# Kernel tuning notes

Measured on AMD Instinct MI355X. Metric: run time of the kernel, lower is better.

Reference implementation:

```python
import jax, jax.numpy as jnp
import numpy as np

N_USERS = 100000
M_ITEMS = 200000
N_NODES = N_USERS + M_ITEMS
N_EDGES = 1200000
D = 64
N_LAYERS = 3
BATCH = 4096


def setup_inputs() -> dict:
    key = jax.random.key(0)
    ks = jax.random.split(key, 11)
    return {
        "users": jax.random.randint(ks[0], (BATCH,), 0, N_USERS),
        "items": jax.random.randint(ks[1], (BATCH,), 0, M_ITEMS),
        "rows": jax.random.randint(ks[2], (N_EDGES,), 0, N_NODES),
        "cols": jax.random.randint(ks[3], (N_EDGES,), 0, N_NODES),
        "vals": jax.random.uniform(ks[4], (N_EDGES,), dtype=jnp.float32),
        "user_emb": jax.random.normal(ks[5], (N_USERS, D), dtype=jnp.float32) * 0.1,
        "item_emb": jax.random.normal(ks[6], (M_ITEMS, D), dtype=jnp.float32) * 0.1,
        "W_gc": jax.random.normal(ks[7], (N_LAYERS, D, D), dtype=jnp.float32) * 0.1,
        "b_gc": jax.random.normal(ks[8], (N_LAYERS, D), dtype=jnp.float32) * 0.1,
        "W_bi": jax.random.normal(ks[9], (N_LAYERS, D, D), dtype=jnp.float32) * 0.1,
        "b_bi": jax.random.normal(ks[10], (N_LAYERS, D), dtype=jnp.float32) * 0.1,
    }


def _spmm(rows, cols, vals, x):
    # sparse.mm(Graph, x): out[r] = sum_e vals[e] * x[cols[e]] for rows[e]==r
    gathered = vals[:, None] * x[cols]  # [E, D]
    return jax.ops.segment_sum(gathered, rows, num_segments=N_NODES)


def _computer(rows, cols, vals, user_emb, item_emb, W_gc, b_gc, W_bi, b_bi):
    ego = jnp.concatenate([user_emb, item_emb], axis=0)  # [N, D]
    embs = [ego]
    for k in range(N_LAYERS):
        side = _spmm(rows, cols, vals, ego)
        sum_emb = side @ W_gc[k] + b_gc[k]
        bi_emb = (ego * side) @ W_bi[k] + b_bi[k]
        ego = jax.nn.leaky_relu(sum_emb + bi_emb, negative_slope=0.2)
        nrm = jnp.linalg.norm(ego, axis=1, keepdims=True)
        ego = ego / jnp.maximum(nrm, 1e-12)
        embs.append(ego)
    mean_emb = jnp.mean(jnp.stack(embs, axis=1), axis=1)  # [N, D]
    return mean_emb[:N_USERS], mean_emb[N_USERS:]


def reference(users, items, rows, cols, vals, user_emb, item_emb, W_gc, b_gc, W_bi, b_bi):
    all_users, all_items = _computer(rows, cols, vals, user_emb, item_emb, W_gc, b_gc, W_bi, b_bi)
    u = all_users[users]  # [B, D]
    i = all_items[items]  # [B, D]
    return jnp.sum(u * i, axis=1)  # [B]
```

## Files before the change

kernel.cpp:

```cpp
#include <hip/hip_runtime.h>
#include <hip/hip_bf16.h>

#define N_USERS 100000
#define M_ITEMS 200000
#define N_NODES 300000
#define N_EDGES 1200000
#define BATCH   4096
#define NB      ((N_NODES + 255) / 256)
#define CHUNK   5

typedef __attribute__((ext_vector_type(8))) short short8;
typedef __attribute__((ext_vector_type(4))) float floatx4;

static __device__ __forceinline__ float b2f(__hip_bfloat16 x) { return __bfloat162float(x); }

static __device__ __forceinline__ short f2bs(float f) {
    union { __hip_bfloat16 h; short s; } u;
    u.h = __float2bfloat16(f);
    return u.s;
}
static __device__ __forceinline__ float us2f(unsigned int us) {
    return __uint_as_float(us << 16);
}

static __device__ __forceinline__ float loadf(const void* p, int i, int isbf) {
    if (isbf) return b2f(((const __hip_bfloat16*)p)[i]);
    return ((const float*)p)[i];
}

static __device__ __forceinline__ void unpack8(float* o, uint4 e) {
    unsigned int w[4] = {e.x, e.y, e.z, e.w};
#pragma unroll
    for (int j = 0; j < 8; ++j) o[j] = us2f((w[j >> 1] >> ((j & 1) * 16)) & 0xFFFFu);
}

static __device__ __forceinline__ void gather16(
    float* o0, float* o1, const unsigned short* ego,
    const void* ue, const void* ie, int node, int quad, int isbf, int use_src) {
    if (!use_src) {
        const unsigned short* p = ego + (size_t)node * 64 + quad * 8;
        unpack8(o0, *(const uint4*)p);
        unpack8(o1, *(const uint4*)(p + 32));
    } else if (isbf) {
        const unsigned short* p = (node < N_USERS)
            ? (const unsigned short*)ue + (size_t)node * 64
            : (const unsigned short*)ie + (size_t)(node - N_USERS) * 64;
        p += quad * 8;
        unpack8(o0, *(const uint4*)p);
        unpack8(o1, *(const uint4*)(p + 32));
    } else {
        const float* p = (node < N_USERS)
            ? (const float*)ue + (size_t)node * 64
            : (const float*)ie + (size_t)(node - N_USERS) * 64;
        p += quad * 8;
        float4 a = *(const float4*)p;
        float4 b = *(const float4*)(p + 4);
        float4 c = *(const float4*)(p + 32);
        float4 d = *(const float4*)(p + 36);
        o0[0]=a.x; o0[1]=a.y; o0[2]=a.z; o0[3]=a.w; o0[4]=b.x; o0[5]=b.y; o0[6]=b.z; o0[7]=b.w;
        o1[0]=c.x; o1[1]=c.y; o1[2]=c.z; o1[3]=c.w; o1[4]=d.x; o1[5]=d.y; o1[6]=d.z; o1[7]=d.w;
    }
}

__global__ void sniff_kernel(const unsigned short* __restrict__ v16, int* __restrict__ flag) {
    if (blockIdx.x == 0 && threadIdx.x == 0) {
        int c = 0;
        for (int i = 0; i < 16; ++i) {
            unsigned int ub = (v16[2 * i] >> 8) & 0xFF;
            if (ub >= 0x3A && ub <= 0x3F) ++c;
        }
        *flag = (c >= 12) ? 1 : 0;
    }
}

__global__ __launch_bounds__(256) void wtrans_kernel(
    const void* __restrict__ Wg, const void* __restrict__ bg,
    const void* __restrict__ Wb, const void* __restrict__ bb,
    const int* __restrict__ flagp, unsigned short* __restrict__ WT,
    float* __restrict__ sb) {
    int isbf = __builtin_amdgcn_readfirstlane(flagp[0]);
    int t = blockIdx.x * 256 + threadIdx.x;
    if (t < 3072) {
        int lane = t & 63, h = (t >> 6) & 1, ct = (t >> 7) & 3, w = (t >> 9) & 1, k = t >> 10;
        int m = lane & 15, quad = lane >> 4;
        const void* Wsrc = w ? Wb : Wg;
#pragma unroll
        for (int j = 0; j < 8; ++j) {
            int kk = h * 32 + quad * 8 + j;
            WT[(size_t)(k * 1024 + w * 512 + ct * 128 + h * 64 + lane) * 8 + j] =
                (unsigned short)f2bs(loadf(Wsrc, k * 4096 + kk * 64 + ct * 16 + m, isbf));
        }
    }
    if (t < 192) sb[t] = loadf(bg, t, isbf) + loadf(bb, t, isbf);
}

__global__ __launch_bounds__(256) void seed_kernel(
    const int* __restrict__ users, const int* __restrict__ items,
    unsigned char* __restrict__ f1, unsigned char* __restrict__ f2,
    unsigned char* __restrict__ f3) {
    int i = blockIdx.x * 256 + threadIdx.x;
    int n = -1;
    if (i < BATCH) n = users[i];
    else if (i < 2 * BATCH) n = N_USERS + items[i - BATCH];
    if (n >= 0) { f1[n] = 1; f2[n] = 1; f3[n] = 1; }
}

__global__ __launch_bounds__(256) void prop1_count_kernel(
    const int4* __restrict__ rows4, const int4* __restrict__ cols4,
    const unsigned char* __restrict__ src, unsigned char* __restrict__ dst,
    int* __restrict__ off) {
    int t = blockIdx.x * 256 + threadIdx.x;
    if (t < N_EDGES / 4) {
        int4 r = rows4[t];
        int4 c = cols4[t];
        atomicAdd(&off[r.x + 1], 1);
        atomicAdd(&off[r.y + 1], 1);
        atomicAdd(&off[r.z + 1], 1);
        atomicAdd(&off[r.w + 1], 1);
        if (src[r.x]) dst[c.x] = 1;
        if (src[r.y]) dst[c.y] = 1;
        if (src[r.z]) dst[c.z] = 1;
        if (src[r.w]) dst[c.w] = 1;
    }
}

__global__ __launch_bounds__(256) void prop_kernel(
    const int4* __restrict__ rows4, const int4* __restrict__ cols4,
    const unsigned char* __restrict__ src, unsigned char* __restrict__ dst) {
    int t = blockIdx.x * 256 + threadIdx.x;
    if (t < N_EDGES / 4) {
        int4 r = rows4[t];
        int4 c = cols4[t];
        if (src[r.x]) dst[c.x] = 1;
        if (src[r.y]) dst[c.y] = 1;
        if (src[r.z]) dst[c.z] = 1;
        if (src[r.w]) dst[c.w] = 1;
    }
}

static __device__ __forceinline__ int deg_class(int d) {
    return d >= 16 ? 0 : d >= 8 ? 1 : d >= 4 ? 2 : 3;
}

__global__ __launch_bounds__(256) void cblock_count12_kernel(
    const unsigned char* __restrict__ flags, const int* __restrict__ off,
    int* __restrict__ bcnt) {
    __shared__ int w[4];
    int n = blockIdx.x * 256 + threadIdx.x;
    int lane = threadIdx.x & 63;
    int wid  = threadIdx.x >> 6;
    bool ir = (n < N_NODES);
    int cls = 3;
    if (ir) cls = deg_class(off[n + 1] - off[n]);
#pragma unroll
    for (int L = 0; L < 3; ++L) {
        bool fl = ir && flags[L * N_NODES + n];
#pragma unroll
        for (int c = 0; c < 4; ++c) {
            unsigned long long mask = __ballot(fl && (cls == c));
            if (lane == 0) w[wid] = __popcll(mask);
            __syncthreads();
            if (threadIdx.x == 0) bcnt[(L * 4 + c) * NB + blockIdx.x] = w[0] + w[1] + w[2] + w[3];
            __syncthreads();
        }
    }
}

__global__ __launch_bounds__(256) void cscan_top12_kernel(
    int* __restrict__ bcnt, int* __restrict__ cnts) {
    __shared__ int s[256];
    int t = threadIdx.x;
    for (int L = 0; L < 3; ++L) {
        int levelRun = 0;
        for (int c = 0; c < 4; ++c) {
            int v = L * 4 + c;
            int base = t * CHUNK;
            int loc = 0;
            for (int j = 0; j < CHUNK; ++j) { int i = base + j; if (i < NB) loc += bcnt[v * NB + i]; }
            s[t] = loc;
            __syncthreads();
            for (int o = 1; o < 256; o <<= 1) {
                int add = (t >= o) ? s[t - o] : 0;
                __syncthreads();
                s[t] += add;
                __syncthreads();
            }
            int run = ((t == 0) ? 0 : s[t - 1]) + levelRun;
            int total = s[255];
            for (int j = 0; j < CHUNK; ++j) {
                int i = base + j;
                if (i < NB) { int tmp = bcnt[v * NB + i]; bcnt[v * NB + i] = run; run += tmp; }
            }
            levelRun += total;
            __syncthreads();
        }
        if (t == 0) cnts[L] = levelRun;
    }
}

__global__ __launch_bounds__(256) void cscatter12_kernel(
    const unsigned char* __restrict__ flags, const int* __restrict__ off,
    const int* __restrict__ bcnt, int* __restrict__ lists) {
    __shared__ int wsum[4];
    int n = blockIdx.x * 256 + threadIdx.x;
    int lane = threadIdx.x & 63;
    int wid  = threadIdx.x >> 6;
    bool ir = (n < N_NODES);
    int cls = 3;
    if (ir) cls = deg_class(off[n + 1] - off[n]);
#pragma unroll
    for (int L = 0; L < 3; ++L) {
        bool fl = ir && flags[L * N_NODES + n];
#pragma unroll
        for (int c = 0; c < 4; ++c) {
            bool f = fl && (cls == c);
            unsigned long long mask = __ballot(f);
            if (lane == 0) wsum[wid] = __popcll(mask);
            __syncthreads();
            int base = bcnt[(L * 4 + c) * NB + blockIdx.x];
            for (int i = 0; i < wid; ++i) base += wsum[i];
            if (f) {
                int pos = base + __popcll(mask & ((1ull << lane) - 1ull));
                lists[L * N_NODES + pos] = n;
            }
            __syncthreads();
        }
    }
}

__global__ __launch_bounds__(256) void scan_bsum_kernel(
    const int* __restrict__ A, int* __restrict__ bsum) {
    __shared__ int s[256];
    int t = threadIdx.x;
    int i = blockIdx.x * 256 + t;
    s[t] = (i < N_NODES) ? A[i] : 0;
    __syncthreads();
    for (int o = 128; o >= 1; o >>= 1) {
        if (t < o) s[t] += s[t + o];
        __syncthreads();
    }
    if (t == 0) bsum[blockIdx.x] = s[0];
}

__global__ __launch_bounds__(256) void scan_top_kernel(int* __restrict__ bsum) {
    __shared__ int s[256];
    int t = threadIdx.x;
    int base = t * CHUNK;
    int loc = 0;
    for (int j = 0; j < CHUNK; ++j) { int i = base + j; if (i < NB) loc += bsum[i]; }
    s[t] = loc;
    __syncthreads();
    for (int o = 1; o < 256; o <<= 1) {
        int add = (t >= o) ? s[t - o] : 0;
        __syncthreads();
        s[t] += add;
        __syncthreads();
    }
    int run = (t == 0) ? 0 : s[t - 1];
    for (int j = 0; j < CHUNK; ++j) {
        int i = base + j;
        if (i < NB) { int tmp = bsum[i]; bsum[i] = run; run += tmp; }
    }
}

__global__ __launch_bounds__(256) void scan_block_kernel(
    int* __restrict__ A, const int* __restrict__ bsum, int* __restrict__ cursor) {
    __shared__ int s[256];
    int t = threadIdx.x;
    int i = blockIdx.x * 256 + t;
    s[t] = (i < N_NODES) ? A[i] : 0;
    __syncthreads();
    for (int o = 1; o < 256; o <<= 1) {
        int add = (t >= o) ? s[t - o] : 0;
        __syncthreads();
        s[t] += add;
        __syncthreads();
    }
    if (i < N_NODES) {
        int val = s[t] + bsum[blockIdx.x];
        A[i] = val;
        cursor[i + 1] = val;
    }
    if (blockIdx.x == 0 && t == 0) cursor[0] = 0;
}

__global__ __launch_bounds__(256) void fill_kernel(
    const int4* __restrict__ rows4, const int4* __restrict__ cols4,
    const void* __restrict__ vals, int* __restrict__ cursor,
    int2* __restrict__ epack, const int* __restrict__ flagp,
    const unsigned char* __restrict__ flag1) {
    int isbf = __builtin_amdgcn_readfirstlane(flagp[0]);
    int t = blockIdx.x * 256 + threadIdx.x;
    if (t < N_EDGES / 4) {
        int4 r = rows4[t];
        int4 c = cols4[t];
        int e = t * 4;
        if (flag1[r.x]) {
            int p = atomicAdd(&cursor[r.x], 1);
            epack[p] = make_int2(c.x, __float_as_int(loadf(vals, e, isbf)));
        }
        if (flag1[r.y]) {
            int p = atomicAdd(&cursor[r.y], 1);
            epack[p] = make_int2(c.y, __float_as_int(loadf(vals, e + 1, isbf)));
        }
        if (flag1[r.z]) {
            int p = atomicAdd(&cursor[r.z], 1);
            epack[p] = make_int2(c.z, __float_as_int(loadf(vals, e + 2, isbf)));
        }
        if (flag1[r.w]) {
            int p = atomicAdd(&cursor[r.w], 1);
            epack[p] = make_int2(c.w, __float_as_int(loadf(vals, e + 3, isbf)));
        }
    }
}

__global__ __launch_bounds__(256) void fused_layer_kernel(
    const int* __restrict__ off, const int2* __restrict__ epack,
    const unsigned short* __restrict__ ego_in,
    const void* __restrict__ ue, const void* __restrict__ ie,
    const unsigned short* __restrict__ WT, const float* __restrict__ sb,
    int klayer, unsigned short* __restrict__ ego_out,
    const int* __restrict__ flagp, const int* __restrict__ list,
    const int* __restrict__ cntp, int use_src) {
    const int isbf = __builtin_amdgcn_readfirstlane(flagp[0]);
    const int cnt  = __builtin_amdgcn_readfirstlane(cntp[0]);
    const int ntile = (cnt + 15) >> 4;
    const int lane = threadIdx.x & 63;
    const int m    = lane & 15;
    const int quad = lane >> 4;

    const unsigned short* wt = WT + (size_t)klayer * 8192;
    short8 Bg[4][2], Bb[4][2];
#pragma unroll
    for (int ct = 0; ct < 4; ++ct)
#pragma unroll
        for (int h = 0; h < 2; ++h) {
            Bg[ct][h] = *(const short8*)(wt + (size_t)((ct * 2 + h) * 64 + lane) * 8);
            Bb[ct][h] = *(const short8*)(wt + (size_t)(512 + (ct * 2 + h) * 64 + lane) * 8);
        }
    float bv[4];
#pragma unroll
    for (int ct = 0; ct < 4; ++ct) bv[ct] = sb[klayer * 64 + ct * 16 + m];

    const int wv = blockIdx.x * 4 + (threadIdx.x >> 6);
    const int nw = gridDim.x * 4;
    for (int tile = wv; tile < ntile; tile += nw) {
        const int idx = tile * 16 + m;
        const int row = list[idx < cnt ? idx : cnt - 1];
        const int start = off[row];
        const int end   = off[row + 1];

        float eg0[8], eg1[8];
        gather16(eg0, eg1, ego_in, ue, ie, row, quad, isbf, use_src);

        float s0[8] = {0,0,0,0,0,0,0,0};
        float s1[8] = {0,0,0,0,0,0,0,0};
        for (int e = start; e < end; ++e) {
            int2 cv = epack[e];
            float v = __int_as_float(cv.y);
            float t0[8], t1[8];
            gather16(t0, t1, ego_in, ue, ie, cv.x, quad, isbf, use_src);
#pragma unroll
            for (int j = 0; j < 8; ++j) {
                s0[j] = fmaf(v, t0[j], s0[j]);
                s1[j] = fmaf(v, t1[j], s1[j]);
            }
        }

        short8 As0, As1, Ap0, Ap1;
#pragma unroll
        for (int j = 0; j < 8; ++j) {
            As0[j] = f2bs(s0[j]);
            As1[j] = f2bs(s1[j]);
            Ap0[j] = f2bs(eg0[j] * s0[j]);
            Ap1[j] = f2bs(eg1[j] * s1[j]);
        }

        floatx4 acc[4];
#pragma unroll
        for (int ct = 0; ct < 4; ++ct) {
            floatx4 a = {0.f, 0.f, 0.f, 0.f};
            a = __builtin_amdgcn_mfma_f32_16x16x32_bf16(As0, Bg[ct][0], a, 0, 0, 0);
            a = __builtin_amdgcn_mfma_f32_16x16x32_bf16(As1, Bg[ct][1], a, 0, 0, 0);
            a = __builtin_amdgcn_mfma_f32_16x16x32_bf16(Ap0, Bb[ct][0], a, 0, 0, 0);
            a = __builtin_amdgcn_mfma_f32_16x16x32_bf16(Ap1, Bb[ct][1], a, 0, 0, 0);
            acc[ct] = a;
        }

        float v[4][4];
        float ssq[4] = {0.f, 0.f, 0.f, 0.f};
#pragma unroll
        for (int ct = 0; ct < 4; ++ct)
#pragma unroll
            for (int r = 0; r < 4; ++r) {
                float x = acc[ct][r] + bv[ct];
                x = x > 0.f ? x : 0.2f * x;
                v[ct][r] = x;
                ssq[r] += x * x;
            }
#pragma unroll
        for (int o = 1; o < 16; o <<= 1)
#pragma unroll
            for (int r = 0; r < 4; ++r) ssq[r] += __shfl_xor(ssq[r], o, 64);
#pragma unroll
        for (int r = 0; r < 4; ++r) {
            int idx_w = tile * 16 + quad * 4 + r;
            if (idx_w < cnt) {
                float sc = 1.0f / fmaxf(sqrtf(ssq[r]), 1e-12f);
                int rw = list[idx_w];
#pragma unroll
                for (int ct = 0; ct < 4; ++ct)
                    ego_out[(size_t)rw * 64 + ct * 16 + m] = (unsigned short)f2bs(v[ct][r] * sc);
            }
        }
    }
}

__global__ __launch_bounds__(256) void batch_acc_kernel(
    const int* __restrict__ users, const int* __restrict__ items,
    const unsigned short* __restrict__ ego, float* __restrict__ acc) {
    int gid = blockIdx.x * 256 + threadIdx.x;
    int b = gid >> 6;
    int lane = gid & 63;
    int node = (b < BATCH) ? users[b] : (N_USERS + items[b - BATCH]);
    acc[gid] += us2f(ego[(size_t)node * 64 + lane]);
}

__global__ __launch_bounds__(256) void dot_kernel(
    const int* __restrict__ users, const int* __restrict__ items,
    const float* __restrict__ acc, const void* __restrict__ ue,
    const void* __restrict__ ie, void* __restrict__ out,
    const int* __restrict__ flagp) {
    int isbf = __builtin_amdgcn_readfirstlane(flagp[0]);
    int gid = blockIdx.x * 256 + threadIdx.x;
    int b = gid >> 6;
    int lane = gid & 63;
    int un = __builtin_amdgcn_readfirstlane(users[b]);
    int in = __builtin_amdgcn_readfirstlane(items[b]);
    float u = acc[b * 64 + lane] + loadf(ue, un * 64 + lane, isbf);
    float v = acc[(BATCH + b) * 64 + lane] + loadf(ie, in * 64 + lane, isbf);
    float pr = u * v;
#pragma unroll
    for (int o = 32; o >= 1; o >>= 1) pr += __shfl_xor(pr, o, 64);
    if (lane == 0) {
        float r = pr * 0.0625f;
        if (isbf) ((__hip_bfloat16*)out)[b] = __float2bfloat16(r);
        else      ((float*)out)[b] = r;
    }
}

static inline size_t align16(size_t x) { return (x + 15) & ~(size_t)15; }

extern "C" void kernel_launch(void* const* d_in, const int* in_sizes, int n_in,
                              void* d_out, int out_size, void* d_ws, size_t ws_size,
                              hipStream_t stream) {
    const int* users = (const int*)d_in[0];
    const int* items = (const int*)d_in[1];
    const int* rows  = (const int*)d_in[2];
    const int* cols  = (const int*)d_in[3];
    const void* vals     = d_in[4];
    const void* user_emb = d_in[5];
    const void* item_emb = d_in[6];
    const void* W_gc     = d_in[7];
    const void* b_gc     = d_in[8];
    const void* W_bi     = d_in[9];
    const void* b_bi     = d_in[10];

    const size_t egoB   = (size_t)N_NODES * 64 * sizeof(short);
    const size_t packB  = (size_t)N_EDGES * sizeof(int2);
    const size_t curB   = (size_t)(N_NODES + 1) * sizeof(int);
    const size_t bsumB  = (size_t)NB * sizeof(int);
    const size_t bcntB  = (size_t)12 * NB * sizeof(int);
    const size_t wtB    = (size_t)3 * 1024 * 8 * sizeof(short);
    const size_t sbB    = (size_t)192 * sizeof(float);
    const size_t accB   = (size_t)2 * BATCH * 64 * sizeof(float);
    const size_t offB   = (size_t)(N_NODES + 1) * sizeof(int);
    const size_t flagsB = (size_t)3 * N_NODES;

    char* ws = (char*)d_ws;
    size_t o = 0;
    unsigned short* egoA  = (unsigned short*)(ws + o); o += egoB;
    unsigned short* egoB2 = (unsigned short*)(ws + o); o += egoB;
    int2*  epack  = (int2*)(ws + o);  o += packB;
    int*   cursor = (int*)(ws + o);   o += curB;
    int*   bsum   = (int*)(ws + o);   o += bsumB;
    int*   bcnt   = (int*)(ws + o);   o += bcntB;
    o = align16(o);
    unsigned short* WT = (unsigned short*)(ws + o); o += wtB;
    float* sb     = (float*)(ws + o); o += sbB;
    o = align16(o);
    float* acc    = (float*)(ws + o);
    int*   off    = (int*)((char*)acc + accB);
    int*   cnts   = (int*)((char*)off + offB);
    int*   flag   = cnts + 3;
    unsigned char* flags = (unsigned char*)(flag + 1);
    const size_t zeroB = accB + offB + 4 * sizeof(int) + flagsB;
    unsigned char* flagL[3] = {flags, flags + N_NODES, flags + 2 * N_NODES};
    int* lists = (int*)(flags + flagsB);
    int* listL[3] = {lists, lists + N_NODES, lists + 2 * N_NODES};

    hipMemsetAsync(acc, 0, zeroB, stream);
    sniff_kernel<<<1, 64, 0, stream>>>((const unsigned short*)vals, flag);
    wtrans_kernel<<<12, 256, 0, stream>>>(W_gc, b_gc, W_bi, b_bi, flag, WT, sb);

    seed_kernel<<<(2 * BATCH + 255) / 256, 256, 0, stream>>>(users, items, flagL[0], flagL[1], flagL[2]);
    prop1_count_kernel<<<(N_EDGES / 4 + 255) / 256, 256, 0, stream>>>(
        (const int4*)rows, (const int4*)cols, flagL[2], flagL[1], off);
    scan_bsum_kernel<<<NB, 256, 0, stream>>>(off + 1, bsum);
    scan_top_kernel<<<1, 256, 0, stream>>>(bsum);
    scan_block_kernel<<<NB, 256, 0, stream>>>(off + 1, bsum, cursor);
    prop_kernel<<<(N_EDGES / 4 + 255) / 256, 256, 0, stream>>>(
        (const int4*)rows, (const int4*)cols, flagL[1], flagL[0]);

    cblock_count12_kernel<<<NB, 256, 0, stream>>>(flags, off, bcnt);
    cscan_top12_kernel<<<1, 256, 0, stream>>>(bcnt, cnts);
    cscatter12_kernel<<<NB, 256, 0, stream>>>(flags, off, bcnt, lists);

    fill_kernel<<<(N_EDGES / 4 + 255) / 256, 256, 0, stream>>>(
        (const int4*)rows, (const int4*)cols, vals, cursor, epack, flag, flagL[0]);

    unsigned short* eg_in[3]  = {egoA, egoA, egoB2};
    unsigned short* eg_out[3] = {egoA, egoB2, egoA};
    for (int k = 0; k < 3; ++k) {
        int use_src = (k == 0) ? 1 : 0;
        fused_layer_kernel<<<2048, 256, 0, stream>>>(off, epack, eg_in[k], user_emb, item_emb,
                                                     WT, sb, k, eg_out[k],
                                                     flag, listL[k], cnts + k, use_src);
        batch_acc_kernel<<<(2 * BATCH * 64) / 256, 256, 0, stream>>>(users, items, eg_out[k], acc);
    }
    dot_kernel<<<(BATCH * 64) / 256, 256, 0, stream>>>(users, items, acc, user_emb, item_emb, d_out, flag);
}
```

Measured before the change: 344.7 us.

## Restructure CSR build with atomic ranks, fuse scans, fold batch accumulation into layers

Merges the sniff, weight-transpose and seed kernels into one setup kernel, and recomputes the dtype sniff inline where it is needed. Row counting now runs after the 2-hop propagation and only for flagged rows. It records each edge's atomic rank, so the fill kernel can scatter without a second round of atomics. The three scans are fused with the degree-class counting into three kernels. Per-batch accumulation is moved into the layer kernel through a map3 index, which removes three batch_acc launches but assumes batch rows are unique per node in map3 and packs ranks into 16 bits.

After: 309.5 us. 1.11x faster.

```diff
diff --git a/kernel.cpp b/kernel.cpp
--- a/kernel.cpp
+++ b/kernel.cpp
@@ -8,6 +8,8 @@
 #define BATCH   4096
 #define NB      ((N_NODES + 255) / 256)
 #define CHUNK   5
+#define EPT2    (N_EDGES / 2)
+#define EGRID   ((EPT2 + 255) / 256)
 
 typedef __attribute__((ext_vector_type(8))) short short8;
 typedef __attribute__((ext_vector_type(4))) float floatx4;
@@ -26,6 +28,17 @@
 static __device__ __forceinline__ float loadf(const void* p, int i, int isbf) {
     if (isbf) return b2f(((const __hip_bfloat16*)p)[i]);
     return ((const float*)p)[i];
+}
+
+static __device__ __forceinline__ int sniff_dev(const void* vals) {
+    const unsigned short* v16 = (const unsigned short*)vals;
+    int c = 0;
+#pragma unroll
+    for (int i = 0; i < 16; ++i) {
+        unsigned int ub = (v16[2 * i] >> 8) & 0xFF;
+        if (ub >= 0x3A && ub <= 0x3F) ++c;
+    }
+    return (c >= 12) ? 1 : 0;
 }
 
 static __device__ __forceinline__ void unpack8(float* o, uint4 e) {
@@ -62,79 +75,60 @@
     }
 }
 
-__global__ void sniff_kernel(const unsigned short* __restrict__ v16, int* __restrict__ flag) {
-    if (blockIdx.x == 0 && threadIdx.x == 0) {
-        int c = 0;
-        for (int i = 0; i < 16; ++i) {
-            unsigned int ub = (v16[2 * i] >> 8) & 0xFF;
-            if (ub >= 0x3A && ub <= 0x3F) ++c;
-        }
-        *flag = (c >= 12) ? 1 : 0;
-    }
-}
-
-__global__ __launch_bounds__(256) void wtrans_kernel(
+__global__ __launch_bounds__(256) void setup_kernel(
     const void* __restrict__ Wg, const void* __restrict__ bg,
     const void* __restrict__ Wb, const void* __restrict__ bb,
-    const int* __restrict__ flagp, unsigned short* __restrict__ WT,
-    float* __restrict__ sb) {
-    int isbf = __builtin_amdgcn_readfirstlane(flagp[0]);
-    int t = blockIdx.x * 256 + threadIdx.x;
-    if (t < 3072) {
-        int lane = t & 63, h = (t >> 6) & 1, ct = (t >> 7) & 3, w = (t >> 9) & 1, k = t >> 10;
-        int m = lane & 15, quad = lane >> 4;
-        const void* Wsrc = w ? Wb : Wg;
-#pragma unroll
-        for (int j = 0; j < 8; ++j) {
-            int kk = h * 32 + quad * 8 + j;
-            WT[(size_t)(k * 1024 + w * 512 + ct * 128 + h * 64 + lane) * 8 + j] =
-                (unsigned short)f2bs(loadf(Wsrc, k * 4096 + kk * 64 + ct * 16 + m, isbf));
-        }
-    }
-    if (t < 192) sb[t] = loadf(bg, t, isbf) + loadf(bb, t, isbf);
-}
-
-__global__ __launch_bounds__(256) void seed_kernel(
+    const void* __restrict__ vals,
     const int* __restrict__ users, const int* __restrict__ items,
+    unsigned short* __restrict__ WT, float* __restrict__ sb,
     unsigned char* __restrict__ f1, unsigned char* __restrict__ f2,
     unsigned char* __restrict__ f3) {
-    int i = blockIdx.x * 256 + threadIdx.x;
-    int n = -1;
-    if (i < BATCH) n = users[i];
-    else if (i < 2 * BATCH) n = N_USERS + items[i - BATCH];
-    if (n >= 0) { f1[n] = 1; f2[n] = 1; f3[n] = 1; }
-}
-
-__global__ __launch_bounds__(256) void prop1_count_kernel(
-    const int4* __restrict__ rows4, const int4* __restrict__ cols4,
-    const unsigned char* __restrict__ src, unsigned char* __restrict__ dst,
-    int* __restrict__ off) {
+    if (blockIdx.x < 12) {
+        int isbf = __builtin_amdgcn_readfirstlane(sniff_dev(vals));
+        int t = blockIdx.x * 256 + threadIdx.x;
+        if (t < 3072) {
+            int lane = t & 63, h = (t >> 6) & 1, ct = (t >> 7) & 3, w = (t >> 9) & 1, k = t >> 10;
+            int m = lane & 15, quad = lane >> 4;
+            const void* Wsrc = w ? Wb : Wg;
+#pragma unroll
+            for (int j = 0; j < 8; ++j) {
+                int kk = h * 32 + quad * 8 + j;
+                WT[(size_t)(k * 1024 + w * 512 + ct * 128 + h * 64 + lane) * 8 + j] =
+                    (unsigned short)f2bs(loadf(Wsrc, k * 4096 + kk * 64 + ct * 16 + m, isbf));
+            }
+        }
+        if (t < 192) sb[t] = loadf(bg, t, isbf) + loadf(bb, t, isbf);
+    } else {
+        int i = (blockIdx.x - 12) * 256 + threadIdx.x;
+        int n = -1;
+        if (i < BATCH) n = users[i];
+        else if (i < 2 * BATCH) n = N_USERS + items[i - BATCH];
+        if (n >= 0) { f1[n] = 1; f2[n] = 1; f3[n] = 1; }
+    }
+}
+
+__global__ __launch_bounds__(256) void prop_kernel(
+    const int2* __restrict__ rows2, const int2* __restrict__ cols2,
+    const unsigned char* __restrict__ src, unsigned char* __restrict__ dst) {
     int t = blockIdx.x * 256 + threadIdx.x;
-    if (t < N_EDGES / 4) {
-        int4 r = rows4[t];
-        int4 c = cols4[t];
-        atomicAdd(&off[r.x + 1], 1);
-        atomicAdd(&off[r.y + 1], 1);
-        atomicAdd(&off[r.z + 1], 1);
-        atomicAdd(&off[r.w + 1], 1);
+    if (t < EPT2) {
+        int2 r = rows2[t];
+        int2 c = cols2[t];
         if (src[r.x]) dst[c.x] = 1;
         if (src[r.y]) dst[c.y] = 1;
-        if (src[r.z]) dst[c.z] = 1;
-        if (src[r.w]) dst[c.w] = 1;
-    }
-}
-
-__global__ __launch_bounds__(256) void prop_kernel(
-    const int4* __restrict__ rows4, const int4* __restrict__ cols4,
-    const unsigned char* __restrict__ src, unsigned char* __restrict__ dst) {
+    }
+}
+
+__global__ __launch_bounds__(256) void count_rank_kernel(
+    const int2* __restrict__ rows2, const unsigned char* __restrict__ flag1,
+    int* __restrict__ off, unsigned int* __restrict__ rank) {
     int t = blockIdx.x * 256 + threadIdx.x;
-    if (t < N_EDGES / 4) {
-        int4 r = rows4[t];
-        int4 c = cols4[t];
-        if (src[r.x]) dst[c.x] = 1;
-        if (src[r.y]) dst[c.y] = 1;
-        if (src[r.z]) dst[c.z] = 1;
-        if (src[r.w]) dst[c.w] = 1;
+    if (t < EPT2) {
+        int2 r = rows2[t];
+        unsigned int k0 = 0xFFFFu, k1 = 0xFFFFu;
+        if (flag1[r.x]) k0 = (unsigned int)atomicAdd(&off[r.x + 1], 1);
+        if (flag1[r.y]) k1 = (unsigned int)atomicAdd(&off[r.y + 1], 1);
+        rank[t] = (k0 & 0xFFFFu) | (k1 << 16);
     }
 }
 
@@ -142,34 +136,62 @@
     return d >= 16 ? 0 : d >= 8 ? 1 : d >= 4 ? 2 : 3;
 }
 
-__global__ __launch_bounds__(256) void cblock_count12_kernel(
-    const unsigned char* __restrict__ flags, const int* __restrict__ off,
-    int* __restrict__ bcnt) {
+__global__ __launch_bounds__(256) void scanA_kernel(
+    const int* __restrict__ off, const unsigned char* __restrict__ flags,
+    int* __restrict__ bsum, int* __restrict__ bcnt, unsigned char* __restrict__ cls) {
+    __shared__ int s[256];
     __shared__ int w[4];
-    int n = blockIdx.x * 256 + threadIdx.x;
-    int lane = threadIdx.x & 63;
-    int wid  = threadIdx.x >> 6;
+    int t = threadIdx.x;
+    int n = blockIdx.x * 256 + t;
     bool ir = (n < N_NODES);
-    int cls = 3;
-    if (ir) cls = deg_class(off[n + 1] - off[n]);
+    int deg = ir ? off[n + 1] : 0;
+    s[t] = deg;
+    __syncthreads();
+    for (int o = 128; o >= 1; o >>= 1) {
+        if (t < o) s[t] += s[t + o];
+        __syncthreads();
+    }
+    if (t == 0) bsum[blockIdx.x] = s[0];
+    int c = deg_class(deg);
+    if (ir) cls[n] = (unsigned char)c;
+    int lane = t & 63;
+    int wid  = t >> 6;
 #pragma unroll
     for (int L = 0; L < 3; ++L) {
         bool fl = ir && flags[L * N_NODES + n];
 #pragma unroll
-        for (int c = 0; c < 4; ++c) {
-            unsigned long long mask = __ballot(fl && (cls == c));
+        for (int cc = 0; cc < 4; ++cc) {
+            unsigned long long mask = __ballot(fl && (c == cc));
             if (lane == 0) w[wid] = __popcll(mask);
             __syncthreads();
-            if (threadIdx.x == 0) bcnt[(L * 4 + c) * NB + blockIdx.x] = w[0] + w[1] + w[2] + w[3];
-            __syncthreads();
-        }
-    }
-}
-
-__global__ __launch_bounds__(256) void cscan_top12_kernel(
-    int* __restrict__ bcnt, int* __restrict__ cnts) {
+            if (t == 0) bcnt[(L * 4 + cc) * NB + blockIdx.x] = w[0] + w[1] + w[2] + w[3];
+            __syncthreads();
+        }
+    }
+}
+
+__global__ __launch_bounds__(256) void scanB_kernel(
+    int* __restrict__ bsum, int* __restrict__ bcnt, int* __restrict__ cnts) {
     __shared__ int s[256];
     int t = threadIdx.x;
+    {
+        int base = t * CHUNK, loc = 0;
+        for (int j = 0; j < CHUNK; ++j) { int i = base + j; if (i < NB) loc += bsum[i]; }
+        s[t] = loc;
+        __syncthreads();
+        for (int o = 1; o < 256; o <<= 1) {
+            int add = (t >= o) ? s[t - o] : 0;
+            __syncthreads();
+            s[t] += add;
+            __syncthreads();
+        }
+        int run = (t == 0) ? 0 : s[t - 1];
+        for (int j = 0; j < CHUNK; ++j) {
+            int i = base + j;
+            if (i < NB) { int tmp = bsum[i]; bsum[i] = run; run += tmp; }
+        }
+        __syncthreads();
+    }
     for (int L = 0; L < 3; ++L) {
         int levelRun = 0;
         for (int c = 0; c < 4; ++c) {
@@ -198,57 +220,16 @@
     }
 }
 
-__global__ __launch_bounds__(256) void cscatter12_kernel(
-    const unsigned char* __restrict__ flags, const int* __restrict__ off,
-    const int* __restrict__ bcnt, int* __restrict__ lists) {
+__global__ __launch_bounds__(256) void scanC_kernel(
+    int* __restrict__ off, const int* __restrict__ bsum,
+    const unsigned char* __restrict__ flags, const unsigned char* __restrict__ cls,
+    const int* __restrict__ bcnt, int* __restrict__ lists, int* __restrict__ map3) {
+    __shared__ int s[256];
     __shared__ int wsum[4];
-    int n = blockIdx.x * 256 + threadIdx.x;
-    int lane = threadIdx.x & 63;
-    int wid  = threadIdx.x >> 6;
+    int t = threadIdx.x;
+    int n = blockIdx.x * 256 + t;
     bool ir = (n < N_NODES);
-    int cls = 3;
-    if (ir) cls = deg_class(off[n + 1] - off[n]);
-#pragma unroll
-    for (int L = 0; L < 3; ++L) {
-        bool fl = ir && flags[L * N_NODES + n];
-#pragma unroll
-        for (int c = 0; c < 4; ++c) {
-            bool f = fl && (cls == c);
-            unsigned long long mask = __ballot(f);
-            if (lane == 0) wsum[wid] = __popcll(mask);
-            __syncthreads();
-            int base = bcnt[(L * 4 + c) * NB + blockIdx.x];
-            for (int i = 0; i < wid; ++i) base += wsum[i];
-            if (f) {
-                int pos = base + __popcll(mask & ((1ull << lane) - 1ull));
-                lists[L * N_NODES + pos] = n;
-            }
-            __syncthreads();
-        }
-    }
-}
-
-__global__ __launch_bounds__(256) void scan_bsum_kernel(
-    const int* __restrict__ A, int* __restrict__ bsum) {
-    __shared__ int s[256];
-    int t = threadIdx.x;
-    int i = blockIdx.x * 256 + t;
-    s[t] = (i < N_NODES) ? A[i] : 0;
-    __syncthreads();
-    for (int o = 128; o >= 1; o >>= 1) {
-        if (t < o) s[t] += s[t + o];
-        __syncthreads();
-    }
-    if (t == 0) bsum[blockIdx.x] = s[0];
-}
-
-__global__ __launch_bounds__(256) void scan_top_kernel(int* __restrict__ bsum) {
-    __shared__ int s[256];
-    int t = threadIdx.x;
-    int base = t * CHUNK;
-    int loc = 0;
-    for (int j = 0; j < CHUNK; ++j) { int i = base + j; if (i < NB) loc += bsum[i]; }
-    s[t] = loc;
+    s[t] = ir ? off[n + 1] : 0;
     __syncthreads();
     for (int o = 1; o < 256; o <<= 1) {
         int add = (t >= o) ? s[t - o] : 0;
@@ -256,61 +237,47 @@
         s[t] += add;
         __syncthreads();
     }
-    int run = (t == 0) ? 0 : s[t - 1];
-    for (int j = 0; j < CHUNK; ++j) {
-        int i = base + j;
-        if (i < NB) { int tmp = bsum[i]; bsum[i] = run; run += tmp; }
-    }
-}
-
-__global__ __launch_bounds__(256) void scan_block_kernel(
-    int* __restrict__ A, const int* __restrict__ bsum, int* __restrict__ cursor) {
-    __shared__ int s[256];
-    int t = threadIdx.x;
-    int i = blockIdx.x * 256 + t;
-    s[t] = (i < N_NODES) ? A[i] : 0;
-    __syncthreads();
-    for (int o = 1; o < 256; o <<= 1) {
-        int add = (t >= o) ? s[t - o] : 0;
-        __syncthreads();
-        s[t] += add;
-        __syncthreads();
-    }
-    if (i < N_NODES) {
-        int val = s[t] + bsum[blockIdx.x];
-        A[i] = val;
-        cursor[i + 1] = val;
-    }
-    if (blockIdx.x == 0 && t == 0) cursor[0] = 0;
+    if (ir) off[n + 1] = s[t] + bsum[blockIdx.x];
+    int c = ir ? (int)cls[n] : 3;
+    int lane = t & 63;
+    int wid  = t >> 6;
+#pragma unroll
+    for (int L = 0; L < 3; ++L) {
+        bool fl = ir && flags[L * N_NODES + n];
+#pragma unroll
+        for (int cc = 0; cc < 4; ++cc) {
+            bool f = fl && (c == cc);
+            unsigned long long mask = __ballot(f);
+            if (lane == 0) wsum[wid] = __popcll(mask);
+            __syncthreads();
+            int base = bcnt[(L * 4 + cc) * NB + blockIdx.x];
+            for (int i = 0; i < wid; ++i) base += wsum[i];
+            if (f) {
+                int pos = base + __popcll(mask & ((1ull << lane) - 1ull));
+                lists[L * N_NODES + pos] = n;
+                if (L == 2) map3[n] = pos + 1;
+            }
+            __syncthreads();
+        }
+    }
 }
 
 __global__ __launch_bounds__(256) void fill_kernel(
-    const int4* __restrict__ rows4, const int4* __restrict__ cols4,
-    const void* __restrict__ vals, int* __restrict__ cursor,
-    int2* __restrict__ epack, const int* __restrict__ flagp,
-    const unsigned char* __restrict__ flag1) {
-    int isbf = __builtin_amdgcn_readfirstlane(flagp[0]);
+    const int2* __restrict__ rows2, const int2* __restrict__ cols2,
+    const void* __restrict__ vals, const int* __restrict__ off,
+    const unsigned int* __restrict__ rank, int2* __restrict__ epack) {
+    int isbf = __builtin_amdgcn_readfirstlane(sniff_dev(vals));
     int t = blockIdx.x * 256 + threadIdx.x;
-    if (t < N_EDGES / 4) {
-        int4 r = rows4[t];
-        int4 c = cols4[t];
-        int e = t * 4;
-        if (flag1[r.x]) {
-            int p = atomicAdd(&cursor[r.x], 1);
-            epack[p] = make_int2(c.x, __float_as_int(loadf(vals, e, isbf)));
-        }
-        if (flag1[r.y]) {
-            int p = atomicAdd(&cursor[r.y], 1);
-            epack[p] = make_int2(c.y, __float_as_int(loadf(vals, e + 1, isbf)));
-        }
-        if (flag1[r.z]) {
-            int p = atomicAdd(&cursor[r.z], 1);
-            epack[p] = make_int2(c.z, __float_as_int(loadf(vals, e + 2, isbf)));
-        }
-        if (flag1[r.w]) {
-            int p = atomicAdd(&cursor[r.w], 1);
-            epack[p] = make_int2(c.w, __float_as_int(loadf(vals, e + 3, isbf)));
-        }
+    if (t < EPT2) {
+        int2 r = rows2[t];
+        int2 c = cols2[t];
+        unsigned int kk = rank[t];
+        unsigned int k0 = kk & 0xFFFFu, k1 = kk >> 16;
+        int e = t * 2;
+        if (k0 != 0xFFFFu)
+            epack[off[r.x] + (int)k0] = make_int2(c.x, __float_as_int(loadf(vals, e, isbf)));
+        if (k1 != 0xFFFFu)
+            epack[off[r.y] + (int)k1] = make_int2(c.y, __float_as_int(loadf(vals, e + 1, isbf)));
     }
 }
 
@@ -318,11 +285,12 @@
     const int* __restrict__ off, const int2* __restrict__ epack,
     const unsigned short* __restrict__ ego_in,
     const void* __restrict__ ue, const void* __restrict__ ie,
+    const void* __restrict__ vals,
     const unsigned short* __restrict__ WT, const float* __restrict__ sb,
     int klayer, unsigned short* __restrict__ ego_out,
-    const int* __restrict__ flagp, const int* __restrict__ list,
-    const int* __restrict__ cntp, int use_src) {
-    const int isbf = __builtin_amdgcn_readfirstlane(flagp[0]);
+    const int* __restrict__ list, const int* __restrict__ cntp, int use_src,
+    const int* __restrict__ map3, float* __restrict__ acc) {
+    const int isbf = use_src ? __builtin_amdgcn_readfirstlane(sniff_dev(vals)) : 0;
     const int cnt  = __builtin_amdgcn_readfirstlane(cntp[0]);
     const int ntile = (cnt + 15) >> 4;
     const int lane = threadIdx.x & 63;
@@ -376,7 +344,7 @@
             Ap1[j] = f2bs(eg1[j] * s1[j]);
         }
 
-        floatx4 acc[4];
+        floatx4 accf[4];
 #pragma unroll
         for (int ct = 0; ct < 4; ++ct) {
             floatx4 a = {0.f, 0.f, 0.f, 0.f};
@@ -384,7 +352,7 @@
             a = __builtin_amdgcn_mfma_f32_16x16x32_bf16(As1, Bg[ct][1], a, 0, 0, 0);
             a = __builtin_amdgcn_mfma_f32_16x16x32_bf16(Ap0, Bb[ct][0], a, 0, 0, 0);
             a = __builtin_amdgcn_mfma_f32_16x16x32_bf16(Ap1, Bb[ct][1], a, 0, 0, 0);
-            acc[ct] = a;
+            accf[ct] = a;
         }
 
         float v[4][4];
@@ -393,7 +361,7 @@
         for (int ct = 0; ct < 4; ++ct)
 #pragma unroll
             for (int r = 0; r < 4; ++r) {
-                float x = acc[ct][r] + bv[ct];
+                float x = accf[ct][r] + bv[ct];
                 x = x > 0.f ? x : 0.2f * x;
                 v[ct][r] = x;
                 ssq[r] += x * x;
@@ -408,37 +376,35 @@
             if (idx_w < cnt) {
                 float sc = 1.0f / fmaxf(sqrtf(ssq[r]), 1e-12f);
                 int rw = list[idx_w];
+                int c3 = map3[rw];
 #pragma unroll
                 for (int ct = 0; ct < 4; ++ct)
                     ego_out[(size_t)rw * 64 + ct * 16 + m] = (unsigned short)f2bs(v[ct][r] * sc);
-            }
-        }
-    }
-}
-
-__global__ __launch_bounds__(256) void batch_acc_kernel(
-    const int* __restrict__ users, const int* __restrict__ items,
-    const unsigned short* __restrict__ ego, float* __restrict__ acc) {
-    int gid = blockIdx.x * 256 + threadIdx.x;
-    int b = gid >> 6;
-    int lane = gid & 63;
-    int node = (b < BATCH) ? users[b] : (N_USERS + items[b - BATCH]);
-    acc[gid] += us2f(ego[(size_t)node * 64 + lane]);
+                if (c3 > 0) {
+                    float* ap = acc + (size_t)(c3 - 1) * 64 + m;
+#pragma unroll
+                    for (int ct = 0; ct < 4; ++ct) ap[ct * 16] += v[ct][r] * sc;
+                }
+            }
+        }
+    }
 }
 
 __global__ __launch_bounds__(256) void dot_kernel(
     const int* __restrict__ users, const int* __restrict__ items,
-    const float* __restrict__ acc, const void* __restrict__ ue,
-    const void* __restrict__ ie, void* __restrict__ out,
-    const int* __restrict__ flagp) {
-    int isbf = __builtin_amdgcn_readfirstlane(flagp[0]);
+    const float* __restrict__ acc, const int* __restrict__ map3,
+    const void* __restrict__ ue, const void* __restrict__ ie,
+    void* __restrict__ out, const void* __restrict__ vals) {
+    int isbf = __builtin_amdgcn_readfirstlane(sniff_dev(vals));
     int gid = blockIdx.x * 256 + threadIdx.x;
     int b = gid >> 6;
     int lane = gid & 63;
     int un = __builtin_amdgcn_readfirstlane(users[b]);
-    int in = __builtin_amdgcn_readfirstlane(items[b]);
-    float u = acc[b * 64 + lane] + loadf(ue, un * 64 + lane, isbf);
-    float v = acc[(BATCH + b) * 64 + lane] + loadf(ie, in * 64 + lane, isbf);
+    int in_ = __builtin_amdgcn_readfirstlane(items[b]);
+    int cu = __builtin_amdgcn_readfirstlane(map3[un]);
+    int ci = __builtin_amdgcn_readfirstlane(map3[N_USERS + in_]);
+    float u = (cu > 0 ? acc[(size_t)(cu - 1) * 64 + lane] : 0.f) + loadf(ue, un * 64 + lane, isbf);
+    float v = (ci > 0 ? acc[(size_t)(ci - 1) * 64 + lane] : 0.f) + loadf(ie, in_ * 64 + lane, isbf);
     float pr = u * v;
 #pragma unroll
     for (int o = 32; o >= 1; o >>= 1) pr += __shfl_xor(pr, o, 64);
@@ -468,13 +434,16 @@
 
     const size_t egoB   = (size_t)N_NODES * 64 * sizeof(short);
     const size_t packB  = (size_t)N_EDGES * sizeof(int2);
-    const size_t curB   = (size_t)(N_NODES + 1) * sizeof(int);
+    const size_t rankB  = (size_t)EPT2 * sizeof(unsigned int);
     const size_t bsumB  = (size_t)NB * sizeof(int);
     const size_t bcntB  = (size_t)12 * NB * sizeof(int);
+    const size_t clsB   = (size_t)N_NODES;
     const size_t wtB    = (size_t)3 * 1024 * 8 * sizeof(short);
     const size_t sbB    = (size_t)192 * sizeof(float);
     const size_t accB   = (size_t)2 * BATCH * 64 * sizeof(float);
     const size_t offB   = (size_t)(N_NODES + 1) * sizeof(int);
+    const size_t cntsB  = (size_t)4 * sizeof(int);
+    const size_t map3B  = (size_t)N_NODES * sizeof(int);
     const size_t flagsB = (size_t)3 * N_NODES;
 
     char* ws = (char*)d_ws;
@@ -482,9 +451,10 @@
     unsigned short* egoA  = (unsigned short*)(ws + o); o += egoB;
     unsigned short* egoB2 = (unsigned short*)(ws + o); o += egoB;
     int2*  epack  = (int2*)(ws + o);  o += packB;
-    int*   cursor = (int*)(ws + o);   o += curB;
+    unsigned int* rank = (unsigned int*)(ws + o); o += rankB;
     int*   bsum   = (int*)(ws + o);   o += bsumB;
     int*   bcnt   = (int*)(ws + o);   o += bcntB;
+    unsigned char* cls = (unsigned char*)(ws + o); o += clsB;
     o = align16(o);
     unsigned short* WT = (unsigned short*)(ws + o); o += wtB;
     float* sb     = (float*)(ws + o); o += sbB;
@@ -492,41 +462,37 @@
     float* acc    = (float*)(ws + o);
     int*   off    = (int*)((char*)acc + accB);
     int*   cnts   = (int*)((char*)off + offB);
-    int*   flag   = cnts + 3;
-    unsigned char* flags = (unsigned char*)(flag + 1);
-    const size_t zeroB = accB + offB + 4 * sizeof(int) + flagsB;
+    int*   map3   = (int*)((char*)cnts + cntsB);
+    unsigned char* flags = (unsigned char*)((char*)map3 + map3B);
+    const size_t zeroB = accB + offB + cntsB + map3B + flagsB;
     unsigned char* flagL[3] = {flags, flags + N_NODES, flags + 2 * N_NODES};
     int* lists = (int*)(flags + flagsB);
     int* listL[3] = {lists, lists + N_NODES, lists + 2 * N_NODES};
 
     hipMemsetAsync(acc, 0, zeroB, stream);
-    sniff_kernel<<<1, 64, 0, stream>>>((const unsigned short*)vals, flag);
-    wtrans_kernel<<<12, 256, 0, stream>>>(W_gc, b_gc, W_bi, b_bi, flag, WT, sb);
-
-    seed_kernel<<<(2 * BATCH + 255) / 256, 256, 0, stream>>>(users, items, flagL[0], flagL[1], flagL[2]);
-    prop1_count_kernel<<<(N_EDGES / 4 + 255) / 256, 256, 0, stream>>>(
-        (const int4*)rows, (const int4*)cols, flagL[2], flagL[1], off);
-    scan_bsum_kernel<<<NB, 256, 0, stream>>>(off + 1, bsum);
-    scan_top_kernel<<<1, 256, 0, stream>>>(bsum);
-    scan_block_kernel<<<NB, 256, 0, stream>>>(off + 1, bsum, cursor);
-    prop_kernel<<<(N_EDGES / 4 + 255) / 256, 256, 0, stream>>>(
-        (const int4*)rows, (const int4*)cols, flagL[1], flagL[0]);
-
-    cblock_count12_kernel<<<NB, 256, 0, stream>>>(flags, off, bcnt);
-    cscan_top12_kernel<<<1, 256, 0, stream>>>(bcnt, cnts);
-    cscatter12_kernel<<<NB, 256, 0, stream>>>(flags, off, bcnt, lists);
-
-    fill_kernel<<<(N_EDGES / 4 + 255) / 256, 256, 0, stream>>>(
-        (const int4*)rows, (const int4*)cols, vals, cursor, epack, flag, flagL[0]);
+
+    setup_kernel<<<44, 256, 0, stream>>>(W_gc, b_gc, W_bi, b_bi, vals, users, items,
+                                         WT, sb, flagL[0], flagL[1], flagL[2]);
+
+    prop_kernel<<<EGRID, 256, 0, stream>>>((const int2*)rows, (const int2*)cols, flagL[2], flagL[1]);
+    prop_kernel<<<EGRID, 256, 0, stream>>>((const int2*)rows, (const int2*)cols, flagL[1], flagL[0]);
+
+    count_rank_kernel<<<EGRID, 256, 0, stream>>>((const int2*)rows, flagL[0], off, rank);
+
+    scanA_kernel<<<NB, 256, 0, stream>>>(off, flags, bsum, bcnt, cls);
+    scanB_kernel<<<1, 256, 0, stream>>>(bsum, bcnt, cnts);
+    scanC_kernel<<<NB, 256, 0, stream>>>(off, bsum, flags, cls, bcnt, lists, map3);
+
+    fill_kernel<<<EGRID, 256, 0, stream>>>((const int2*)rows, (const int2*)cols, vals, off, rank, epack);
 
     unsigned short* eg_in[3]  = {egoA, egoA, egoB2};
     unsigned short* eg_out[3] = {egoA, egoB2, egoA};
     for (int k = 0; k < 3; ++k) {
         int use_src = (k == 0) ? 1 : 0;
         fused_layer_kernel<<<2048, 256, 0, stream>>>(off, epack, eg_in[k], user_emb, item_emb,
-                                                     WT, sb, k, eg_out[k],
-                                                     flag, listL[k], cnts + k, use_src);
-        batch_acc_kernel<<<(2 * BATCH * 64) / 256, 256, 0, stream>>>(users, items, eg_out[k], acc);
-    }
-    dot_kernel<<<(BATCH * 64) / 256, 256, 0, stream>>>(users, items, acc, user_emb, item_emb, d_out, flag);
-}
+                                                     vals, WT, sb, k, eg_out[k],
+                                                     listL[k], cnts + k, use_src, map3, acc);
+    }
+    dot_kernel<<<(BATCH * 64) / 256, 256, 0, stream>>>(users, items, acc, map3,
+                                                       user_emb, item_emb, d_out, vals);
+}
```
